# Performance work log

Hardware: AMD Instinct MI355X
Metric: run time of the kernel (lower is better)

## Reference

```python
import jax, jax.numpy as jnp
import numpy as np

D_MODEL = 512
NHEAD = 8
D_HEAD = D_MODEL // NHEAD
SCALE = D_HEAD ** -0.5
EPS = 1e-8


def setup_inputs() -> dict:
    key = jax.random.key(0)
    ks = jax.random.split(key, 12)
    B, N = 4, 2048
    s = D_MODEL ** -0.5
    return {
        "Q_input": jax.random.normal(ks[0], (B, N, D_MODEL), jnp.float32),
        "KV_input": jax.random.normal(ks[1], (B, N, D_MODEL), jnp.float32),
        "SC": jax.random.uniform(ks[2], (B, N, N), jnp.float32),
        "Wq_w": jax.random.normal(ks[3], (D_MODEL, D_MODEL), jnp.float32) * s,
        "Wq_b": jnp.zeros((D_MODEL,), jnp.float32),
        "Wk_w": jax.random.normal(ks[4], (D_MODEL, D_MODEL), jnp.float32) * s,
        "Wk_b": jnp.zeros((D_MODEL,), jnp.float32),
        "Wv_w": jax.random.normal(ks[5], (D_MODEL, D_MODEL), jnp.float32) * s,
        "Wv_b": jnp.zeros((D_MODEL,), jnp.float32),
        "gate_w": jax.random.normal(ks[6], (), jnp.float32),
        "gate_b": jnp.zeros((), jnp.float32),
        "out_w": jax.random.normal(ks[7], (D_MODEL, D_MODEL), jnp.float32) * s,
        "out_b": jnp.zeros((D_MODEL,), jnp.float32),
    }


def reference(Q_input, KV_input, SC, Wq_w, Wq_b, Wk_w, Wk_b, Wv_w, Wv_b,
              gate_w, gate_b, out_w, out_b):
    B, N, _ = Q_input.shape
    # projections -> [B, H, N, d_head]
    def proj(x, w, b):
        y = x @ w.T + b
        return y.reshape(B, N, NHEAD, D_HEAD).transpose(0, 2, 1, 3)
    Q = proj(Q_input, Wq_w, Wq_b)
    K = proj(KV_input, Wk_w, Wk_b)
    V = proj(KV_input, Wv_w, Wv_b)
    # scores [B, H, N, N]
    scores = jnp.einsum('bhqd,bhkd->bhqk', Q, K) * SCALE
    # per-edge gate: sigmoid(w*SC + b), broadcast over heads
    g = jax.nn.sigmoid(SC * gate_w + gate_b)  # [B, N, N]
    scores = scores + jnp.log(g + EPS)[:, None, :, :]
    attn = jax.nn.softmax(scores, axis=-1)
    out = jnp.einsum('bhqk,bhkd->bhqd', attn, V)
    out = out.transpose(0, 2, 1, 3).reshape(B, N, D_MODEL)
    return out @ out_w.T + out_b
```

## Files before the change

### kernel.cpp

```cpp
#include <hip/hip_runtime.h>

typedef unsigned short u16;
typedef unsigned int u32;
typedef __attribute__((ext_vector_type(4))) float f32x4;
typedef __attribute__((ext_vector_type(8))) short s16x8;
typedef __attribute__((ext_vector_type(4))) u16 u16x4;
typedef __attribute__((ext_vector_type(2))) u32 u32x2;

#define L2E 1.4426950408889634f
#define QSCALE 0.18033688011112042f

__device__ __forceinline__ float bf2f(u16 u) {
    union { u32 i; float f; } v; v.i = ((u32)u) << 16; return v.f;
}
__device__ __forceinline__ u16 f2bf(float f) {
    union { float f; u32 i; } v; v.f = f;
    return (u16)((v.i + 0x7fffu + ((v.i >> 16) & 1u)) >> 16);
}
__device__ __forceinline__ u32 pack_hi(float a, float b) {
    union { float f; u32 i; } x, y; x.f = a; y.f = b;
    return (x.i >> 16) | (y.i & 0xFFFF0000u);
}
__device__ __forceinline__ float bflo(u32 w) {
    union { u32 i; float f; } v; v.i = w << 16; return v.f;
}
__device__ __forceinline__ float bfhi(u32 w) {
    union { u32 i; float f; } v; v.i = w & 0xFFFF0000u; return v.f;
}

__device__ __forceinline__ void gl2lds16(const u16* g, u16* l) {
    __builtin_amdgcn_global_load_lds(
        (const __attribute__((address_space(1))) void*)g,
        (__attribute__((address_space(3))) void*)l, 16, 0, 0);
}

__global__ __launch_bounds__(256) void prep_kernel(
    const float* __restrict__ s0, const float* __restrict__ s1,
    const float* __restrict__ s2, const float* __restrict__ s3,
    const float* __restrict__ s4, const float* __restrict__ s5,
    u16* __restrict__ dst,
    const float* __restrict__ SC, const float* __restrict__ gwp,
    const float* __restrict__ gbp, u16* __restrict__ LGx)
{
    if (blockIdx.x < 9216) {
        int e = (blockIdx.x * 256 + threadIdx.x) * 4;
        const float* src; int off;
        if      (e < 4194304) { src = s0; off = e; }
        else if (e < 8388608) { src = s1; off = e - 4194304; }
        else if (e < 8650752) { src = s2; off = e - 8388608; }
        else if (e < 8912896) { src = s3; off = e - 8650752; }
        else if (e < 9175040) { src = s4; off = e - 8912896; }
        else                  { src = s5; off = e - 9175040; }
        f32x4 f = *(const f32x4*)(src + off);
        u16x4 o;
#pragma unroll
        for (int j = 0; j < 4; ++j) o[j] = f2bf(f[j]);
        *(u16x4*)(dst + e) = o;
    } else {
        const int flat = (blockIdx.x - 9216) * 256 + threadIdx.x;
        const int lane = flat & 63;
        const int kt   = (flat >> 6) & 31;
        const int t16  = (flat >> 11) & 127;
        const int b    = flat >> 18;
        const int l16 = lane & 15, quad = lane >> 4;
        const float tA = -gwp[0] * L2E, tB = -gbp[0] * L2E;
        const float* row = SC + ((size_t)b * 2048 + t16 * 16 + l16) * 2048
                              + kt * 64 + quad * 4;
        __align__(16) u16 tmp[16];
#pragma unroll
        for (int kk = 0; kk < 4; ++kk) {
            f32x4 x = *(const f32x4*)(row + kk * 16);
#pragma unroll
            for (int reg = 0; reg < 4; ++reg) {
                float g = __builtin_amdgcn_rcpf(
                    1.0f + __builtin_amdgcn_exp2f(tA * x[reg] + tB)) + 1e-8f;
                tmp[kk * 4 + reg] = f2bf(__builtin_amdgcn_logf(g));
            }
        }
        u16* d = LGx + (size_t)flat * 16;
        *(uint4*)d       = *(uint4*)tmp;
        *(uint4*)(d + 8) = *(uint4*)(tmp + 8);
    }
}

__device__ __forceinline__ void gemm_core(
    const u16* __restrict__ A, const u16* __restrict__ Bw,
    int m0, int n0, u16* As, u16* Bs, f32x4 acc[4][4])
{
    const int tid = threadIdx.x;
    const int lane = tid & 63, w = tid >> 6;
    const int wm = w >> 1, wn = w & 1;
    const int l16 = lane & 15, quad = lane >> 4;
    const int srow = (lane >> 2), sch = (lane & 3) * 8;
    const f32x4 vzero = {0.f, 0.f, 0.f, 0.f};
#pragma unroll
    for (int i = 0; i < 4; ++i)
#pragma unroll
        for (int j = 0; j < 4; ++j) acc[i][j] = vzero;

#pragma unroll
    for (int j = 0; j < 2; ++j) {
        int row = w * 32 + j * 16 + srow;
        gl2lds16(&A[(size_t)(m0 + row) * 512 + sch], &As[w * 1024 + j * 512]);
        gl2lds16(&Bw[(size_t)(n0 + row) * 512 + sch], &Bs[w * 1024 + j * 512]);
    }
    for (int kt = 0; kt < 16; ++kt) {
        __syncthreads();
        const int cur = (kt & 1) * 4096;
        if (kt < 15) {
            const int nxt = ((kt + 1) & 1) * 4096;
#pragma unroll
            for (int j = 0; j < 2; ++j) {
                int row = w * 32 + j * 16 + srow;
                gl2lds16(&A[(size_t)(m0 + row) * 512 + (kt + 1) * 32 + sch],
                         &As[nxt + w * 1024 + j * 512]);
                gl2lds16(&Bw[(size_t)(n0 + row) * 512 + (kt + 1) * 32 + sch],
                         &Bs[nxt + w * 1024 + j * 512]);
            }
        }
        s16x8 af[4], bfr[4];
#pragma unroll
        for (int mt = 0; mt < 4; ++mt)
            af[mt] = *(const s16x8*)&As[cur + (wm * 64 + mt * 16 + l16) * 32 + quad * 8];
#pragma unroll
        for (int nt = 0; nt < 4; ++nt)
            bfr[nt] = *(const s16x8*)&Bs[cur + (wn * 64 + nt * 16 + l16) * 32 + quad * 8];
#pragma unroll
        for (int mt = 0; mt < 4; ++mt)
#pragma unroll
            for (int nt = 0; nt < 4; ++nt)
                acc[mt][nt] = __builtin_amdgcn_mfma_f32_16x16x32_bf16(
                    af[mt], bfr[nt], acc[mt][nt], 0, 0, 0);
    }
}

__global__ __launch_bounds__(256) void proj_kernel(
    const u16* __restrict__ cQin, const u16* __restrict__ cKV,
    const u16* __restrict__ cW,
    const float* __restrict__ bq, const float* __restrict__ bk,
    const float* __restrict__ bv,
    u16* __restrict__ Qh, u16* __restrict__ Kh, u16* __restrict__ Vt)
{
    __shared__ __align__(16) u16 As[2 * 4096];
    __shared__ __align__(16) u16 Bs[2 * 4096];
    const int job = blockIdx.z;
    const u16* A = (job == 0) ? cQin : cKV;
    const u16* W = cW + (size_t)job * 262144;
    const float* bias = (job == 0) ? bq : (job == 1 ? bk : bv);
    const int m0 = blockIdx.y * 128, n0 = blockIdx.x * 128;
    f32x4 acc[4][4];
    gemm_core(A, W, m0, n0, As, Bs, acc);

    const int tid = threadIdx.x, lane = tid & 63, w = tid >> 6;
    const int wm = w >> 1, wn = w & 1, l16 = lane & 15, quad = lane >> 4;
#pragma unroll
    for (int nt = 0; nt < 4; ++nt) {
        int j = n0 + wn * 64 + nt * 16 + l16;
        float bj = bias[j];
        int h = j >> 6, d = j & 63;
#pragma unroll
        for (int mt = 0; mt < 4; ++mt) {
            int trow = m0 + wm * 64 + mt * 16 + quad * 4;
            int bb = trow >> 11, nn = trow & 2047;
            int bh = bb * 8 + h;
            if (job == 2) {
                u16x4 pv;
#pragma unroll
                for (int reg = 0; reg < 4; ++reg) pv[reg] = f2bf(acc[mt][nt][reg] + bj);
                *(u16x4*)&Vt[(size_t)(bh * 64 + d) * 2048 + nn] = pv;
            } else if (job == 0) {
#pragma unroll
                for (int reg = 0; reg < 4; ++reg)
                    Qh[(size_t)(bh * 2048 + nn + reg) * 64 + d] =
                        f2bf((acc[mt][nt][reg] + bj) * QSCALE);
            } else {
#pragma unroll
                for (int reg = 0; reg < 4; ++reg)
                    Kh[(size_t)(bh * 2048 + nn + reg) * 64 + d] =
                        f2bf(acc[mt][nt][reg] + bj);
            }
        }
    }
}

__global__ __launch_bounds__(512, 4) void attn_kernel(
    const u16* __restrict__ Qh, const u16* __restrict__ Kh,
    const u16* __restrict__ Vt, const u16* __restrict__ LGx,
    u16* __restrict__ Ob)
{
    __shared__ __align__(16) u16 Ks[2][8192];
    __shared__ __align__(16) u16 Vs[2][8192];
    const int tid = threadIdx.x;
    const int w = tid >> 6, lane = tid & 63;
    const int l16 = lane & 15, quad = lane >> 4;
    const int b = blockIdx.z, head = blockIdx.y, qg = blockIdx.x;
    const int bh = b * 8 + head;
    const int q0 = qg * 128 + w * 16;
    const int t16 = qg * 8 + w;
    const u16* Qp = Qh + (size_t)bh * 131072;
    const u16* Kp = Kh + (size_t)bh * 131072;
    const u16* Vp = Vt + (size_t)bh * 131072;
    const u16* LGt = LGx + ((size_t)((b * 128 + t16) * 32) * 64 + lane) * 16;
    const f32x4 vzero = {0.f, 0.f, 0.f, 0.f};
    const s16x8 ones = {0x3F80, 0x3F80, 0x3F80, 0x3F80,
                        0x3F80, 0x3F80, 0x3F80, 0x3F80};

    const int s3 = l16 & 7, s2x = s3 & 3, s4x = s3 & 4;
    const int qsw = (quad ^ s2x) * 8;
    const int kb0 = l16 * 64 + qsw + s4x * 8;
    const int kb1 = l16 * 64 + qsw + (4 ^ s4x) * 8;
    const int vb0 = l16 * 64 + qsw + s4x * 8;
    const int vb1 = l16 * 64 + qsw + (4 ^ s4x) * 8;
    const u16* KbL = &Ks[0][0];
    const u16* VbL = &Vs[0][0];

    const int w4 = w & 3;
    const bool isK = (w < 4);
    const int sr = lane >> 3, c8 = lane & 7;
    const u16* sg0 = isK
        ? (Kp + (size_t)(w4 * 32 + 0 + sr) * 64 + (c8 ^ sr) * 8)
        : (Vp + (size_t)(w4 * 16 + 0 + sr) * 2048 + (c8 ^ sr) * 8);
    const u16* sg1 = isK
        ? (Kp + (size_t)(w4 * 32 + 8 + sr) * 64 + (c8 ^ sr) * 8)
        : (Vp + (size_t)(w4 * 16 + 8 + sr) * 2048 + (c8 ^ sr) * 8);
    const u16* sg2 = isK
        ? (Kp + (size_t)(w4 * 32 + 16 + sr) * 64 + (c8 ^ sr) * 8)
        : (Vp + (size_t)(w4 * 16 + 0 + sr) * 2048 + 64 + (c8 ^ sr) * 8);
    const u16* sg3 = isK
        ? (Kp + (size_t)(w4 * 32 + 24 + sr) * 64 + (c8 ^ sr) * 8)
        : (Vp + (size_t)(w4 * 16 + 8 + sr) * 2048 + 64 + (c8 ^ sr) * 8);
    const size_t sAdv = isK ? 8192 : 128;
    u16* sd0 = isK ? &Ks[0][(w4 * 32 + 0) * 64]  : &Vs[0][(w4 * 16 + 0) * 64];
    u16* sd1 = isK ? &Ks[0][(w4 * 32 + 8) * 64]  : &Vs[0][(w4 * 16 + 8) * 64];
    u16* sd2 = isK ? &Ks[0][(w4 * 32 + 16) * 64] : &Vs[0][4096 + (w4 * 16 + 0) * 64];
    u16* sd3 = isK ? &Ks[0][(w4 * 32 + 24) * 64] : &Vs[0][4096 + (w4 * 16 + 8) * 64];

    s16x8 qf0 = *(const s16x8*)&Qp[(size_t)(q0 + l16) * 64 + quad * 8];
    s16x8 qf1 = *(const s16x8*)&Qp[(size_t)(q0 + l16) * 64 + 32 + quad * 8];
    f32x4 o[4], lacc = vzero;
#pragma unroll
    for (int dn = 0; dn < 4; ++dn) o[dn] = vzero;

    gl2lds16(sg0, sd0); gl2lds16(sg1, sd1);
    gl2lds16(sg2, sd2); gl2lds16(sg3, sd3);
    sg0 += sAdv; sg1 += sAdv; sg2 += sAdv; sg3 += sAdv;
    uint4 lg0 = *(const uint4*)LGt;
    uint4 lg1 = *(const uint4*)(LGt + 8);
    uint4 lg2 = *(const uint4*)(LGt + 1024);
    uint4 lg3 = *(const uint4*)(LGt + 1032);
    const u16* lgP = LGt + 2048;

#define QKHALF(LA, LB, PWB, KOFF)                                              \
    {                                                                          \
        const u32 wdh[8] = {LA.x, LA.y, LA.z, LA.w, LB.x, LB.y, LB.z, LB.w};   \
        _Pragma("unroll")                                                      \
        for (int kk = 0; kk < 4; ++kk) {                                       \
            f32x4 ci;                                                          \
            ci[0] = bflo(wdh[kk * 2]);     ci[1] = bfhi(wdh[kk * 2]);          \
            ci[2] = bflo(wdh[kk * 2 + 1]); ci[3] = bfhi(wdh[kk * 2 + 1]);      \
            s16x8 ka = *(const s16x8*)(KbL + bo + kb0 + (KOFF + kk) * 1024);   \
            s16x8 kb = *(const s16x8*)(KbL + bo + kb1 + (KOFF + kk) * 1024);   \
            f32x4 s = __builtin_amdgcn_mfma_f32_16x16x32_bf16(ka, qf0, ci, 0, 0, 0); \
            s = __builtin_amdgcn_mfma_f32_16x16x32_bf16(kb, qf1, s, 0, 0, 0);  \
            float p0 = __builtin_amdgcn_exp2f(s[0]);                           \
            float p1 = __builtin_amdgcn_exp2f(s[1]);                           \
            float p2 = __builtin_amdgcn_exp2f(s[2]);                           \
            float p3 = __builtin_amdgcn_exp2f(s[3]);                           \
            Pw[PWB + kk][0] = pack_hi(p0, p1);                                 \
            Pw[PWB + kk][1] = pack_hi(p2, p3);                                 \
        }                                                                      \
    }

    for (int kt = 0; kt < 16; ++kt) {
        __syncthreads();
        const int bo = (kt & 1) * 8192;
        if (kt < 15) {
            const int bn = 8192 - bo;
            gl2lds16(sg0, sd0 + bn); gl2lds16(sg1, sd1 + bn);
            gl2lds16(sg2, sd2 + bn); gl2lds16(sg3, sd3 + bn);
            sg0 += sAdv; sg1 += sAdv; sg2 += sAdv; sg3 += sAdv;
        }
        __builtin_amdgcn_s_setprio(1);
        u32 Pw[8][2];
        QKHALF(lg0, lg1, 0, 0);
        QKHALF(lg2, lg3, 4, 4);
        if (kt < 15) {
            lg0 = *(const uint4*)lgP;
            lg1 = *(const uint4*)(lgP + 8);
            lg2 = *(const uint4*)(lgP + 1024);
            lg3 = *(const uint4*)(lgP + 1032);
            lgP += 2048;
        }
#pragma unroll
        for (int kc = 0; kc < 4; ++kc) {
            union { u32 wrd[4]; s16x8 v; } pu;
#pragma unroll
            for (int i = 0; i < 2; ++i) {
                u32x2 r1 = __builtin_amdgcn_permlane32_swap(
                    Pw[2 * kc][i], Pw[2 * kc + 1][i], false, false);
                u32x2 r2 = __builtin_amdgcn_permlane16_swap(
                    r1[0], r1[1], false, false);
                pu.wrd[i]     = r2[0];
                pu.wrd[2 + i] = r2[1];
            }
            s16x8 pf = pu.v;
            lacc = __builtin_amdgcn_mfma_f32_16x16x32_bf16(pf, ones, lacc, 0, 0, 0);
            const int vbb = ((kc & 1) ? vb1 : vb0) + (kc >> 1) * 4096 + bo;
#pragma unroll
            for (int dn = 0; dn < 4; ++dn) {
                s16x8 vf = *(const s16x8*)(VbL + vbb + dn * 1024);
                o[dn] = __builtin_amdgcn_mfma_f32_16x16x32_bf16(
                    pf, vf, o[dn], 0, 0, 0);
            }
        }
        __builtin_amdgcn_s_setprio(0);
    }
#undef QKHALF
#pragma unroll
    for (int reg = 0; reg < 4; ++reg) {
        float inv = __builtin_amdgcn_rcpf(lacc[reg]);
        int trow = b * 2048 + q0 + quad * 4 + reg;
#pragma unroll
        for (int dn = 0; dn < 4; ++dn)
            Ob[(size_t)trow * 512 + head * 64 + dn * 16 + l16] =
                f2bf(o[dn][reg] * inv);
    }
}

__global__ __launch_bounds__(256) void out_kernel(
    const u16* __restrict__ Ob, const u16* __restrict__ cWo,
    const float* __restrict__ bo, float* __restrict__ out)
{
    __shared__ __align__(16) u16 As[2 * 4096];
    __shared__ __align__(16) u16 Bs[2 * 4096];
    const int m0 = blockIdx.y * 128, n0 = blockIdx.x * 128;
    f32x4 acc[4][4];
    gemm_core(Ob, cWo, m0, n0, As, Bs, acc);
    const int tid = threadIdx.x, lane = tid & 63, w = tid >> 6;
    const int wm = w >> 1, wn = w & 1, l16 = lane & 15, quad = lane >> 4;
#pragma unroll
    for (int nt = 0; nt < 4; ++nt) {
        int j = n0 + wn * 64 + nt * 16 + l16;
        float bj = bo[j];
#pragma unroll
        for (int mt = 0; mt < 4; ++mt) {
            int t = m0 + wm * 64 + mt * 16 + quad * 4;
#pragma unroll
            for (int reg = 0; reg < 4; ++reg)
                out[(size_t)(t + reg) * 512 + j] = acc[mt][nt][reg] + bj;
        }
    }
}

extern "C" void kernel_launch(void* const* d_in, const int* in_sizes, int n_in,
                              void* d_out, int out_size, void* d_ws, size_t ws_size,
                              hipStream_t stream)
{
    const float* Qin  = (const float*)d_in[0];
    const float* KVin = (const float*)d_in[1];
    const float* SC   = (const float*)d_in[2];
    const float* Wq   = (const float*)d_in[3];
    const float* bq   = (const float*)d_in[4];
    const float* Wk   = (const float*)d_in[5];
    const float* bk   = (const float*)d_in[6];
    const float* Wv   = (const float*)d_in[7];
    const float* bv   = (const float*)d_in[8];
    const float* gw   = (const float*)d_in[9];
    const float* gb   = (const float*)d_in[10];
    const float* Wo   = (const float*)d_in[11];
    const float* bo   = (const float*)d_in[12];
    float* out = (float*)d_out;

    u16* conv = (u16*)d_ws;
    u16* cQin = conv;
    u16* cKV  = conv + 4194304;
    u16* cW   = conv + 8388608;
    u16* Qh   = conv + 9437184;
    u16* Kh   = Qh + 4194304;
    u16* Vt   = Kh + 4194304;
    u16* Ob   = Vt + 4194304;
    u16* LGx  = Ob + 4194304;

    hipLaunchKernelGGL(prep_kernel, dim3(13312), dim3(256), 0, stream,
                       Qin, KVin, Wq, Wk, Wv, Wo, conv, SC, gw, gb, LGx);
    hipLaunchKernelGGL(proj_kernel, dim3(4, 64, 3), dim3(256), 0, stream,
                       cQin, cKV, cW, bq, bk, bv, Qh, Kh, Vt);
    hipLaunchKernelGGL(attn_kernel, dim3(16, 8, 4), dim3(512), 0, stream,
                       Qh, Kh, Vt, LGx, Ob);
    hipLaunchKernelGGL(out_kernel, dim3(4, 64), dim3(256), 0, stream,
                       Ob, cW + 786432, bo, out);
}
```

Baseline: 237.0 us.

## Process two query tiles per wave to reuse K/V LDS fragments

The attention kernel drops from 8 to 4 waves per block, and each wave now handles two 16-row query tiles instead of one. K and V fragments read from LDS are shared across both tiles' MFMAs, halving LDS read traffic per unit of compute and adding more independent MFMA chains for latency hiding. Staging is reorganized so 2 waves load K and 2 load V with 8 async copies each. The cost is roughly doubled accumulator and P registers per wave and fewer waves per block, which may reduce occupancy.

```diff
diff --git a/kernel.cpp b/kernel.cpp
--- a/kernel.cpp
+++ b/kernel.cpp
@@ -10,9 +10,6 @@
 #define L2E 1.4426950408889634f
 #define QSCALE 0.18033688011112042f
 
-__device__ __forceinline__ float bf2f(u16 u) {
-    union { u32 i; float f; } v; v.i = ((u32)u) << 16; return v.f;
-}
 __device__ __forceinline__ u16 f2bf(float f) {
     union { float f; u32 i; } v; v.f = f;
     return (u16)((v.i + 0x7fffu + ((v.i >> 16) & 1u)) >> 16);
@@ -183,7 +180,7 @@
     }
 }
 
-__global__ __launch_bounds__(512, 4) void attn_kernel(
+__global__ __launch_bounds__(256, 2) void attn_kernel(
     const u16* __restrict__ Qh, const u16* __restrict__ Kh,
     const u16* __restrict__ Vt, const u16* __restrict__ LGx,
     u16* __restrict__ Ob)
@@ -195,79 +192,82 @@
     const int l16 = lane & 15, quad = lane >> 4;
     const int b = blockIdx.z, head = blockIdx.y, qg = blockIdx.x;
     const int bh = b * 8 + head;
-    const int q0 = qg * 128 + w * 16;
-    const int t16 = qg * 8 + w;
+    const int q0a = qg * 128 + w * 32, q0b = q0a + 16;
+    const int t16a = qg * 8 + w * 2;
     const u16* Qp = Qh + (size_t)bh * 131072;
     const u16* Kp = Kh + (size_t)bh * 131072;
     const u16* Vp = Vt + (size_t)bh * 131072;
-    const u16* LGt = LGx + ((size_t)((b * 128 + t16) * 32) * 64 + lane) * 16;
+    const u16* lgPa = LGx + ((size_t)((b * 128 + t16a) * 32) * 64 + lane) * 16;
+    const u16* lgPb = LGx + ((size_t)((b * 128 + t16a + 1) * 32) * 64 + lane) * 16;
     const f32x4 vzero = {0.f, 0.f, 0.f, 0.f};
     const s16x8 ones = {0x3F80, 0x3F80, 0x3F80, 0x3F80,
                         0x3F80, 0x3F80, 0x3F80, 0x3F80};
 
     const int s3 = l16 & 7, s2x = s3 & 3, s4x = s3 & 4;
     const int qsw = (quad ^ s2x) * 8;
-    const int kb0 = l16 * 64 + qsw + s4x * 8;
-    const int kb1 = l16 * 64 + qsw + (4 ^ s4x) * 8;
-    const int vb0 = l16 * 64 + qsw + s4x * 8;
-    const int vb1 = l16 * 64 + qsw + (4 ^ s4x) * 8;
+    const int rb0 = l16 * 64 + qsw + s4x * 8;
+    const int rb1 = l16 * 64 + qsw + (4 ^ s4x) * 8;
     const u16* KbL = &Ks[0][0];
     const u16* VbL = &Vs[0][0];
 
-    const int w4 = w & 3;
-    const bool isK = (w < 4);
     const int sr = lane >> 3, c8 = lane & 7;
-    const u16* sg0 = isK
-        ? (Kp + (size_t)(w4 * 32 + 0 + sr) * 64 + (c8 ^ sr) * 8)
-        : (Vp + (size_t)(w4 * 16 + 0 + sr) * 2048 + (c8 ^ sr) * 8);
-    const u16* sg1 = isK
-        ? (Kp + (size_t)(w4 * 32 + 8 + sr) * 64 + (c8 ^ sr) * 8)
-        : (Vp + (size_t)(w4 * 16 + 8 + sr) * 2048 + (c8 ^ sr) * 8);
-    const u16* sg2 = isK
-        ? (Kp + (size_t)(w4 * 32 + 16 + sr) * 64 + (c8 ^ sr) * 8)
-        : (Vp + (size_t)(w4 * 16 + 0 + sr) * 2048 + 64 + (c8 ^ sr) * 8);
-    const u16* sg3 = isK
-        ? (Kp + (size_t)(w4 * 32 + 24 + sr) * 64 + (c8 ^ sr) * 8)
-        : (Vp + (size_t)(w4 * 16 + 8 + sr) * 2048 + 64 + (c8 ^ sr) * 8);
-    const size_t sAdv = isK ? 8192 : 128;
-    u16* sd0 = isK ? &Ks[0][(w4 * 32 + 0) * 64]  : &Vs[0][(w4 * 16 + 0) * 64];
-    u16* sd1 = isK ? &Ks[0][(w4 * 32 + 8) * 64]  : &Vs[0][(w4 * 16 + 8) * 64];
-    u16* sd2 = isK ? &Ks[0][(w4 * 32 + 16) * 64] : &Vs[0][4096 + (w4 * 16 + 0) * 64];
-    u16* sd3 = isK ? &Ks[0][(w4 * 32 + 24) * 64] : &Vs[0][4096 + (w4 * 16 + 8) * 64];
-
-    s16x8 qf0 = *(const s16x8*)&Qp[(size_t)(q0 + l16) * 64 + quad * 8];
-    s16x8 qf1 = *(const s16x8*)&Qp[(size_t)(q0 + l16) * 64 + 32 + quad * 8];
-    f32x4 o[4], lacc = vzero;
-#pragma unroll
-    for (int dn = 0; dn < 4; ++dn) o[dn] = vzero;
-
-    gl2lds16(sg0, sd0); gl2lds16(sg1, sd1);
-    gl2lds16(sg2, sd2); gl2lds16(sg3, sd3);
-    sg0 += sAdv; sg1 += sAdv; sg2 += sAdv; sg3 += sAdv;
-    uint4 lg0 = *(const uint4*)LGt;
-    uint4 lg1 = *(const uint4*)(LGt + 8);
-    uint4 lg2 = *(const uint4*)(LGt + 1024);
-    uint4 lg3 = *(const uint4*)(LGt + 1032);
-    const u16* lgP = LGt + 2048;
-
-#define QKHALF(LA, LB, PWB, KOFF)                                              \
+    const bool isK = (w < 2);
+    const int hv = w & 1;
+    const u16* sgq = isK
+        ? (Kp + (size_t)(hv * 64 + sr) * 64 + (c8 ^ sr) * 8)
+        : (Vp + (size_t)sr * 2048 + hv * 64 + (c8 ^ sr) * 8);
+    const size_t slabAdv = isK ? 512 : 16384;
+    const size_t tileAdv = isK ? 8192 : 128;
+    u16* sdb = isK ? &Ks[0][hv * 4096] : &Vs[0][hv * 4096];
+
+    s16x8 qfa0 = *(const s16x8*)&Qp[(size_t)(q0a + l16) * 64 + quad * 8];
+    s16x8 qfa1 = *(const s16x8*)&Qp[(size_t)(q0a + l16) * 64 + 32 + quad * 8];
+    s16x8 qfb0 = *(const s16x8*)&Qp[(size_t)(q0b + l16) * 64 + quad * 8];
+    s16x8 qfb1 = *(const s16x8*)&Qp[(size_t)(q0b + l16) * 64 + 32 + quad * 8];
+    f32x4 oA[4], oB[4], laccA = vzero, laccB = vzero;
+#pragma unroll
+    for (int dn = 0; dn < 4; ++dn) { oA[dn] = vzero; oB[dn] = vzero; }
+
+#pragma unroll
+    for (int j = 0; j < 8; ++j)
+        gl2lds16(sgq + (size_t)j * slabAdv, sdb + j * 512);
+    sgq += tileAdv;
+    uint4 lga0 = *(const uint4*)lgPa;
+    uint4 lga1 = *(const uint4*)(lgPa + 8);
+    uint4 lga2 = *(const uint4*)(lgPa + 1024);
+    uint4 lga3 = *(const uint4*)(lgPa + 1032);
+    uint4 lgb0 = *(const uint4*)lgPb;
+    uint4 lgb1 = *(const uint4*)(lgPb + 8);
+    uint4 lgb2 = *(const uint4*)(lgPb + 1024);
+    uint4 lgb3 = *(const uint4*)(lgPb + 1032);
+    lgPa += 2048; lgPb += 2048;
+
+#define QKQUAD(LA, LB, MA, MB, KOFF)                                           \
     {                                                                          \
-        const u32 wdh[8] = {LA.x, LA.y, LA.z, LA.w, LB.x, LB.y, LB.z, LB.w};   \
+        const u32 wda[8] = {LA.x, LA.y, LA.z, LA.w, LB.x, LB.y, LB.z, LB.w};   \
+        const u32 wdb[8] = {MA.x, MA.y, MA.z, MA.w, MB.x, MB.y, MB.z, MB.w};   \
         _Pragma("unroll")                                                      \
         for (int kk = 0; kk < 4; ++kk) {                                       \
+            s16x8 ka = *(const s16x8*)(KbL + bo + rb0 + (KOFF + kk) * 1024);   \
+            s16x8 kb = *(const s16x8*)(KbL + bo + rb1 + (KOFF + kk) * 1024);   \
             f32x4 ci;                                                          \
-            ci[0] = bflo(wdh[kk * 2]);     ci[1] = bfhi(wdh[kk * 2]);          \
-            ci[2] = bflo(wdh[kk * 2 + 1]); ci[3] = bfhi(wdh[kk * 2 + 1]);      \
-            s16x8 ka = *(const s16x8*)(KbL + bo + kb0 + (KOFF + kk) * 1024);   \
-            s16x8 kb = *(const s16x8*)(KbL + bo + kb1 + (KOFF + kk) * 1024);   \
-            f32x4 s = __builtin_amdgcn_mfma_f32_16x16x32_bf16(ka, qf0, ci, 0, 0, 0); \
-            s = __builtin_amdgcn_mfma_f32_16x16x32_bf16(kb, qf1, s, 0, 0, 0);  \
-            float p0 = __builtin_amdgcn_exp2f(s[0]);                           \
-            float p1 = __builtin_amdgcn_exp2f(s[1]);                           \
-            float p2 = __builtin_amdgcn_exp2f(s[2]);                           \
-            float p3 = __builtin_amdgcn_exp2f(s[3]);                           \
-            Pw[PWB + kk][0] = pack_hi(p0, p1);                                 \
-            Pw[PWB + kk][1] = pack_hi(p2, p3);                                 \
+            ci[0] = bflo(wda[kk * 2]);     ci[1] = bfhi(wda[kk * 2]);          \
+            ci[2] = bflo(wda[kk * 2 + 1]); ci[3] = bfhi(wda[kk * 2 + 1]);      \
+            f32x4 s = __builtin_amdgcn_mfma_f32_16x16x32_bf16(ka, qfa0, ci, 0, 0, 0); \
+            s = __builtin_amdgcn_mfma_f32_16x16x32_bf16(kb, qfa1, s, 0, 0, 0); \
+            f32x4 cj;                                                          \
+            cj[0] = bflo(wdb[kk * 2]);     cj[1] = bfhi(wdb[kk * 2]);          \
+            cj[2] = bflo(wdb[kk * 2 + 1]); cj[3] = bfhi(wdb[kk * 2 + 1]);      \
+            f32x4 t = __builtin_amdgcn_mfma_f32_16x16x32_bf16(ka, qfb0, cj, 0, 0, 0); \
+            t = __builtin_amdgcn_mfma_f32_16x16x32_bf16(kb, qfb1, t, 0, 0, 0); \
+            PwA[KOFF + kk][0] = pack_hi(__builtin_amdgcn_exp2f(s[0]),          \
+                                        __builtin_amdgcn_exp2f(s[1]));         \
+            PwA[KOFF + kk][1] = pack_hi(__builtin_amdgcn_exp2f(s[2]),          \
+                                        __builtin_amdgcn_exp2f(s[3]));         \
+            PwB[KOFF + kk][0] = pack_hi(__builtin_amdgcn_exp2f(t[0]),          \
+                                        __builtin_amdgcn_exp2f(t[1]));         \
+            PwB[KOFF + kk][1] = pack_hi(__builtin_amdgcn_exp2f(t[2]),          \
+                                        __builtin_amdgcn_exp2f(t[3]));         \
         }                                                                      \
     }
 
@@ -275,55 +275,74 @@
         __syncthreads();
         const int bo = (kt & 1) * 8192;
         if (kt < 15) {
-            const int bn = 8192 - bo;
-            gl2lds16(sg0, sd0 + bn); gl2lds16(sg1, sd1 + bn);
-            gl2lds16(sg2, sd2 + bn); gl2lds16(sg3, sd3 + bn);
-            sg0 += sAdv; sg1 += sAdv; sg2 += sAdv; sg3 += sAdv;
+            u16* dd = sdb + (8192 - bo);
+#pragma unroll
+            for (int j = 0; j < 8; ++j)
+                gl2lds16(sgq + (size_t)j * slabAdv, dd + j * 512);
+            sgq += tileAdv;
         }
         __builtin_amdgcn_s_setprio(1);
-        u32 Pw[8][2];
-        QKHALF(lg0, lg1, 0, 0);
-        QKHALF(lg2, lg3, 4, 4);
+        u32 PwA[8][2], PwB[8][2];
+        QKQUAD(lga0, lga1, lgb0, lgb1, 0);
+        QKQUAD(lga2, lga3, lgb2, lgb3, 4);
         if (kt < 15) {
-            lg0 = *(const uint4*)lgP;
-            lg1 = *(const uint4*)(lgP + 8);
-            lg2 = *(const uint4*)(lgP + 1024);
-            lg3 = *(const uint4*)(lgP + 1032);
-            lgP += 2048;
+            lga0 = *(const uint4*)lgPa;
+            lga1 = *(const uint4*)(lgPa + 8);
+            lga2 = *(const uint4*)(lgPa + 1024);
+            lga3 = *(const uint4*)(lgPa + 1032);
+            lgb0 = *(const uint4*)lgPb;
+            lgb1 = *(const uint4*)(lgPb + 8);
+            lgb2 = *(const uint4*)(lgPb + 1024);
+            lgb3 = *(const uint4*)(lgPb + 1032);
+            lgPa += 2048; lgPb += 2048;
         }
 #pragma unroll
         for (int kc = 0; kc < 4; ++kc) {
-            union { u32 wrd[4]; s16x8 v; } pu;
+            union { u32 wrd[4]; s16x8 v; } pa, pb;
 #pragma unroll
             for (int i = 0; i < 2; ++i) {
                 u32x2 r1 = __builtin_amdgcn_permlane32_swap(
-                    Pw[2 * kc][i], Pw[2 * kc + 1][i], false, false);
+                    PwA[2 * kc][i], PwA[2 * kc + 1][i], false, false);
                 u32x2 r2 = __builtin_amdgcn_permlane16_swap(
                     r1[0], r1[1], false, false);
-                pu.wrd[i]     = r2[0];
-                pu.wrd[2 + i] = r2[1];
+                pa.wrd[i]     = r2[0];
+                pa.wrd[2 + i] = r2[1];
+                u32x2 r3 = __builtin_amdgcn_permlane32_swap(
+                    PwB[2 * kc][i], PwB[2 * kc + 1][i], false, false);
+                u32x2 r4 = __builtin_amdgcn_permlane16_swap(
+                    r3[0], r3[1], false, false);
+                pb.wrd[i]     = r4[0];
+                pb.wrd[2 + i] = r4[1];
             }
-            s16x8 pf = pu.v;
-            lacc = __builtin_amdgcn_mfma_f32_16x16x32_bf16(pf, ones, lacc, 0, 0, 0);
-            const int vbb = ((kc & 1) ? vb1 : vb0) + (kc >> 1) * 4096 + bo;
+            s16x8 pfa = pa.v, pfb = pb.v;
+            laccA = __builtin_amdgcn_mfma_f32_16x16x32_bf16(pfa, ones, laccA, 0, 0, 0);
+            laccB = __builtin_amdgcn_mfma_f32_16x16x32_bf16(pfb, ones, laccB, 0, 0, 0);
+            const int vbb = ((kc & 1) ? rb1 : rb0) + (kc >> 1) * 4096 + bo;
 #pragma unroll
             for (int dn = 0; dn < 4; ++dn) {
                 s16x8 vf = *(const s16x8*)(VbL + vbb + dn * 1024);
-                o[dn] = __builtin_amdgcn_mfma_f32_16x16x32_bf16(
-                    pf, vf, o[dn], 0, 0, 0);
+                oA[dn] = __builtin_amdgcn_mfma_f32_16x16x32_bf16(
+                    pfa, vf, oA[dn], 0, 0, 0);
+                oB[dn] = __builtin_amdgcn_mfma_f32_16x16x32_bf16(
+                    pfb, vf, oB[dn], 0, 0, 0);
             }
         }
         __builtin_amdgcn_s_setprio(0);
     }
-#undef QKHALF
+#undef QKQUAD
 #pragma unroll
     for (int reg = 0; reg < 4; ++reg) {
-        float inv = __builtin_amdgcn_rcpf(lacc[reg]);
-        int trow = b * 2048 + q0 + quad * 4 + reg;
-#pragma unroll
-        for (int dn = 0; dn < 4; ++dn)
-            Ob[(size_t)trow * 512 + head * 64 + dn * 16 + l16] =
-                f2bf(o[dn][reg] * inv);
+        float invA = __builtin_amdgcn_rcpf(laccA[reg]);
+        float invB = __builtin_amdgcn_rcpf(laccB[reg]);
+        int trowA = b * 2048 + q0a + quad * 4 + reg;
+        int trowB = b * 2048 + q0b + quad * 4 + reg;
+#pragma unroll
+        for (int dn = 0; dn < 4; ++dn) {
+            Ob[(size_t)trowA * 512 + head * 64 + dn * 16 + l16] =
+                f2bf(oA[dn][reg] * invA);
+            Ob[(size_t)trowB * 512 + head * 64 + dn * 16 + l16] =
+                f2bf(oB[dn][reg] * invB);
+        }
     }
 }
 
@@ -385,7 +404,7 @@
                        Qin, KVin, Wq, Wk, Wv, Wo, conv, SC, gw, gb, LGx);
     hipLaunchKernelGGL(proj_kernel, dim3(4, 64, 3), dim3(256), 0, stream,
                        cQin, cKV, cW, bq, bk, bv, Qh, Kh, Vt);
-    hipLaunchKernelGGL(attn_kernel, dim3(16, 8, 4), dim3(512), 0, stream,
+    hipLaunchKernelGGL(attn_kernel, dim3(16, 8, 4), dim3(256), 0, stream,
                        Qh, Kh, Vt, LGx, Ob);
     hipLaunchKernelGGL(out_kernel, dim3(4, 64), dim3(256), 0, stream,
                        Ob, cW + 786432, bo, out);
```

Result: no change. 239.0 us (+0.8%).
